# Kernel optimization log

Hardware: AMD Instinct MI355X
Metric: run time of the kernel (lower is better)

The kernel has to match this reference:

```python
import jax, jax.numpy as jnp
import numpy as np

KH = KW = 3
K = KH * KW
GROUPS = 8


def conv_same(x, w, b=None):
    out = jax.lax.conv_general_dilated(x, w, (1, 1), 'SAME',
                                       dimension_numbers=('NHWC', 'HWIO', 'NHWC'))
    if b is not None:
        out = out + b
    return out


def feature_selection(x, w_att, w_sel):
    pooled = x.mean(axis=(1, 2), keepdims=True)            # [B,1,1,C]
    attn = jax.nn.sigmoid(conv_same(pooled, w_att))        # 1x1 conv, sigmoid
    return conv_same(x * (attn + 1.0), w_sel)              # [B,H,W,F]


def deform_sample(x, sy, sx):
    # x: [H,W,G,Cg]; sy,sx: [H,W,G,K] fractional sample coords (zero outside)
    H, W, G, _ = x.shape
    y0 = jnp.floor(sy)
    x0 = jnp.floor(sx)
    wy1 = sy - y0
    wx1 = sx - x0
    gi = jnp.arange(G)[None, None, :, None]

    def gather(yi, xi):
        valid = (yi >= 0) & (yi <= H - 1) & (xi >= 0) & (xi <= W - 1)
        yc = jnp.clip(yi, 0, H - 1).astype(jnp.int32)
        xc = jnp.clip(xi, 0, W - 1).astype(jnp.int32)
        v = x[yc, xc, gi]                                   # [H,W,G,K,Cg]
        return v * valid[..., None]

    v00 = gather(y0, x0)
    v01 = gather(y0, x0 + 1)
    v10 = gather(y0 + 1, x0)
    v11 = gather(y0 + 1, x0 + 1)
    wy1 = wy1[..., None]
    wx1 = wx1[..., None]
    top = v00 * (1 - wx1) + v01 * wx1
    bot = v10 * (1 - wx1) + v11 * wx1
    return top * (1 - wy1) + bot * wy1                      # [H,W,G,K,Cg]


def dcnv2(x, align, w_om, b_om, w_dcn, b_dcn):
    # x: [B,H,W,C] input to deform-conv; align: [B,H,W,Ca] alignment feature
    B, H, W, C = x.shape
    G = GROUPS
    Cg = C // G
    om = conv_same(align, w_om, b_om)                       # [B,H,W,G*3*K]
    off = om[..., :G * 2 * K].reshape(B, H, W, G, K, 2)     # (dy, dx)
    mask = jax.nn.sigmoid(om[..., G * 2 * K:]).reshape(B, H, W, G, K)

    iy = jnp.arange(H, dtype=x.dtype)[:, None, None, None]
    ix = jnp.arange(W, dtype=x.dtype)[None, :, None, None]
    ky, kx = jnp.meshgrid(jnp.arange(KH) - (KH - 1) // 2,
                          jnp.arange(KW) - (KW - 1) // 2, indexing='ij')
    ky = ky.reshape(K).astype(x.dtype)
    kx = kx.reshape(K).astype(x.dtype)
    sy = iy + ky + off[..., 0]                              # [B,H,W,G,K]
    sx = ix + kx + off[..., 1]

    xg = x.reshape(B, H, W, G, Cg)
    sampled = jax.vmap(deform_sample)(xg, sy, sx)           # [B,H,W,G,K,Cg]
    sampled = sampled * mask[..., None]
    sampled = sampled.transpose(0, 1, 2, 4, 3, 5).reshape(B, H, W, K, C)
    wk = w_dcn.reshape(K, C, -1)                            # [K,C,F]
    return jnp.einsum('bhwkc,kcf->bhwf', sampled, wk) + b_dcn


def reference(coarse, fine, w_att, w_sel, w_off, w_om, b_om, w_dcn, b_dcn):
    B, H, W, _ = fine.shape
    coarse_up = jax.image.resize(coarse, (B, H, W, coarse.shape[-1]), 'bilinear')
    fine_cal = feature_selection(fine, w_att, w_sel)
    fc = jnp.concatenate([fine_cal, coarse_up * 2.0], axis=-1)
    align = conv_same(fc, w_off)                            # 1x1, no bias
    aligned = jax.nn.relu(dcnv2(coarse_up, align, w_om, b_om, w_dcn, b_dcn))
    return aligned + fine_cal


def setup_inputs() -> dict:
    key = jax.random.key(0)
    ks = jax.random.split(key, 8)
    B, H, W = 4, 64, 64
    Cc, Cf, F = 256, 256, 256
    s = lambda fan: (2.0 / fan) ** 0.5
    return {
        'coarse': jax.random.normal(ks[0], (B, H // 2, W // 2, Cc), jnp.float32),
        'fine': jax.random.normal(ks[1], (B, H, W, Cf), jnp.float32),
        'w_att': jax.random.normal(ks[2], (1, 1, Cf, Cf), jnp.float32) * s(Cf),
        'w_sel': jax.random.normal(ks[3], (1, 1, Cf, F), jnp.float32) * s(Cf),
        'w_off': jax.random.normal(ks[4], (1, 1, F + Cc, 2 * F), jnp.float32) * s(F + Cc),
        'w_om': jax.random.normal(ks[5], (3, 3, 2 * F, GROUPS * 3 * K), jnp.float32) * 0.01,
        'b_om': jnp.zeros((GROUPS * 3 * K,), jnp.float32),
        'w_dcn': jax.random.normal(ks[6], (3, 3, Cc, F), jnp.float32) * s(9 * Cc),
        'b_dcn': jnp.zeros((F,), jnp.float32),
    }
```

## Files before the change

kernel.cpp:

```cpp
#include <hip/hip_runtime.h>
#include <hip/hip_bf16.h>
#include <cstddef>

constexpr int HWP = 64 * 64;
constexpr int CCH = 256;
constexpr int OMC = 216;
constexpr int KDC = 2304;

typedef __attribute__((ext_vector_type(8))) short bf16x8;
typedef __attribute__((ext_vector_type(4))) float f32x4;

__device__ inline unsigned short f2bf(float x) {
  __hip_bfloat16 h = __float2bfloat16(x);
  return *reinterpret_cast<unsigned short*>(&h);
}
__device__ inline float bf2f(unsigned short u) {
  unsigned int v = ((unsigned int)u) << 16;
  return __uint_as_float(v);
}
__device__ inline void bfpair(unsigned int u, float& a, float& b) {
  a = __uint_as_float(u << 16);
  b = __uint_as_float(u & 0xffff0000u);
}

__global__ __launch_bounds__(256) void prep_transpose(
    const float* __restrict__ w_off, const float* __restrict__ w_om,
    const float* __restrict__ w_sel, const float* __restrict__ w_dcn,
    unsigned short* __restrict__ w_offT, unsigned short* __restrict__ w_omT,
    unsigned short* __restrict__ w_selT, unsigned short* __restrict__ w_dcnT) {
  __shared__ float tile[32][33];
  int bid = blockIdx.x;
  int t = threadIdx.x;
  const float* src;
  unsigned short* dst;
  int in_rs, out_rs, r0, c0, cmax;
  if (bid < 256) {
    int tr = bid >> 4, tc = bid & 15;
    src = w_off; dst = w_offT; in_rs = 512; out_rs = 512;
    r0 = tr * 32; c0 = tc * 32; cmax = 512;
  } else if (bid < 320) {
    int b2 = bid - 256;
    int tr = b2 >> 3, tc = b2 & 7;
    src = w_sel; dst = w_selT; in_rs = 256; out_rs = 256;
    r0 = tr * 32; c0 = tc * 32; cmax = 256;
  } else if (bid < 896) {
    int b2 = bid - 320;
    int tap = b2 >> 6; b2 &= 63;
    int tr = b2 >> 3, tc = b2 & 7;
    src = w_dcn + (size_t)tap * 65536; dst = w_dcnT + (size_t)tap * 65536;
    in_rs = 256; out_rs = 256;
    r0 = tr * 32; c0 = tc * 32; cmax = 256;
  } else {
    int b2 = bid - 896;
    int tap = b2 >> 7; b2 &= 127;
    int tr = b2 >> 3, tc = b2 & 7;
    src = w_om + (size_t)tap * 512 * 216; dst = w_omT + (size_t)tap * 256 * 512;
    in_rs = 216; out_rs = 512;
    r0 = tr * 32; c0 = tc * 32; cmax = 216;
  }
  int row = t >> 3, c4 = (t & 7) * 4;
#pragma unroll
  for (int j = 0; j < 4; ++j) {
    int cc = c0 + c4 + j;
    tile[row][c4 + j] = (cc < cmax) ? src[(size_t)(r0 + row) * in_rs + cc] : 0.f;
  }
  __syncthreads();
  ushort4 v;
  v.x = f2bf(tile[c4 + 0][row]);
  v.y = f2bf(tile[c4 + 1][row]);
  v.z = f2bf(tile[c4 + 2][row]);
  v.w = f2bf(tile[c4 + 3][row]);
  *(ushort4*)&dst[(size_t)(c0 + row) * out_rs + r0 + c4] = v;
}

__global__ __launch_bounds__(256) void pool_partial(
    const float* __restrict__ fine, float* __restrict__ partial) {
  int r = blockIdx.x;
  int b = blockIdx.y;
  int t = threadIdx.x;
  const float* src = fine + ((size_t)b * 4096 + r * 64) * 256 + t;
  float s = 0.f;
#pragma unroll 8
  for (int p = 0; p < 64; ++p) s += src[(size_t)p * 256];
  partial[((size_t)b * 64 + r) * 256 + t] = s;
}

__global__ __launch_bounds__(256) void pool_finish(
    const float* __restrict__ partial, const float* __restrict__ w_att,
    float* __restrict__ scale) {
  __shared__ float pl[256];
  int b = blockIdx.x;
  int t = threadIdx.x;
  const float* pp = partial + (size_t)b * 64 * 256 + t;
  float s = 0.f;
#pragma unroll 8
  for (int r = 0; r < 64; ++r) s += pp[(size_t)r * 256];
  pl[t] = s * (1.0f / 4096.0f);
  __syncthreads();
  float acc = 0.f;
  for (int ci = 0; ci < 256; ++ci) acc += pl[ci] * w_att[ci * 256 + t];
  scale[b * 256 + t] = 1.0f + 1.0f / (1.0f + expf(-acc));
}

__global__ __launch_bounds__(256) void upsample_kernel(
    const float* __restrict__ coarse, unsigned short* __restrict__ upbf,
    unsigned short* __restrict__ alignA) {
  int m = blockIdx.x;
  int c = threadIdx.x;
  int b = m >> 12, h = (m >> 6) & 63, w = m & 63;
  float cy = fminf(fmaxf(h * 0.5f - 0.25f, 0.f), 31.f);
  float cx = fminf(fmaxf(w * 0.5f - 0.25f, 0.f), 31.f);
  int y0 = (int)cy, x0 = (int)cx;
  float fy = cy - y0, fx = cx - x0;
  int y1 = min(y0 + 1, 31), x1 = min(x0 + 1, 31);
  const float* base = coarse + (size_t)b * 32 * 32 * CCH;
  float v00 = base[(y0 * 32 + x0) * CCH + c];
  float v01 = base[(y0 * 32 + x1) * CCH + c];
  float v10 = base[(y1 * 32 + x0) * CCH + c];
  float v11 = base[(y1 * 32 + x1) * CCH + c];
  float top = v00 + (v01 - v00) * fx;
  float bot = v10 + (v11 - v10) * fx;
  float v = top + (bot - top) * fy;
  upbf[(size_t)m * CCH + c] = f2bf(v);
  alignA[(size_t)m * 512 + 256 + c] = f2bf(2.f * v);
}

__global__ __launch_bounds__(256) void gemm_finecal_mfma(
    const float* __restrict__ fine, const float* __restrict__ scale,
    const unsigned short* __restrict__ w_selT,
    float* __restrict__ finecal, unsigned short* __restrict__ alignA) {
  __shared__ unsigned short As[128][72];
  __shared__ unsigned short Bs[64][72];
  __shared__ float sc[256];
  int n0 = blockIdx.x * 64;
  int m0 = blockIdx.y * 128;
  int t = threadIdx.x;
  int wid = t >> 6, lane = t & 63;
  int lrow = lane & 15, lq = lane >> 4;
  int bb = m0 >> 12;
  sc[t] = scale[bb * 256 + t];
  f32x4 acc[2][4];
#pragma unroll
  for (int i = 0; i < 2; ++i)
#pragma unroll
    for (int j = 0; j < 4; ++j) acc[i][j] = (f32x4){0.f, 0.f, 0.f, 0.f};
  for (int k0 = 0; k0 < 256; k0 += 64) {
    __syncthreads();
    for (int u = t; u < 128 * 8; u += 256) {
      int row = u >> 3, ck = u & 7;
      const float* fp = &fine[(size_t)(m0 + row) * 256 + k0 + ck * 8];
      float4 f0 = *(const float4*)fp;
      float4 f1 = *(const float4*)(fp + 4);
      int kb = k0 + ck * 8;
      ushort4 u0 = make_ushort4(f2bf(f0.x * sc[kb]), f2bf(f0.y * sc[kb + 1]),
                                f2bf(f0.z * sc[kb + 2]), f2bf(f0.w * sc[kb + 3]));
      ushort4 u1 = make_ushort4(f2bf(f1.x * sc[kb + 4]), f2bf(f1.y * sc[kb + 5]),
                                f2bf(f1.z * sc[kb + 6]), f2bf(f1.w * sc[kb + 7]));
      *(ushort4*)&As[row][ck * 8] = u0;
      *(ushort4*)&As[row][ck * 8 + 4] = u1;
    }
    for (int u = t; u < 64 * 8; u += 256) {
      int row = u >> 3, ck = u & 7;
      *(uint4*)&Bs[row][ck * 8] = *(const uint4*)&w_selT[(size_t)(n0 + row) * 256 + k0 + ck * 8];
    }
    __syncthreads();
#pragma unroll
    for (int kk = 0; kk < 2; ++kk) {
      bf16x8 a[2], b[4];
#pragma unroll
      for (int mt = 0; mt < 2; ++mt)
        a[mt] = *(const bf16x8*)&As[wid * 32 + mt * 16 + lrow][kk * 32 + lq * 8];
#pragma unroll
      for (int nt = 0; nt < 4; ++nt)
        b[nt] = *(const bf16x8*)&Bs[nt * 16 + lrow][kk * 32 + lq * 8];
#pragma unroll
      for (int mt = 0; mt < 2; ++mt)
#pragma unroll
        for (int nt = 0; nt < 4; ++nt)
          acc[mt][nt] = __builtin_amdgcn_mfma_f32_16x16x32_bf16(
              a[mt], b[nt], acc[mt][nt], 0, 0, 0);
    }
  }
#pragma unroll
  for (int mt = 0; mt < 2; ++mt)
#pragma unroll
    for (int nt = 0; nt < 4; ++nt)
#pragma unroll
      for (int r = 0; r < 4; ++r) {
        int m = m0 + wid * 32 + mt * 16 + lq * 4 + r;
        int n = n0 + nt * 16 + lrow;
        finecal[(size_t)m * 256 + n] = acc[mt][nt][r];
        alignA[(size_t)m * 512 + n] = f2bf(acc[mt][nt][r]);
      }
}

__global__ __launch_bounds__(256) void gemm_align_mfma(
    const unsigned short* __restrict__ alignA,
    const unsigned short* __restrict__ w_offT,
    unsigned short* __restrict__ alignBf) {
  __shared__ unsigned short As[128][72];
  __shared__ unsigned short Bs[64][72];
  int n0 = blockIdx.x * 64;
  int m0 = blockIdx.y * 128;
  int t = threadIdx.x;
  int wid = t >> 6, lane = t & 63;
  int lrow = lane & 15, lq = lane >> 4;
  f32x4 acc[2][4];
#pragma unroll
  for (int i = 0; i < 2; ++i)
#pragma unroll
    for (int j = 0; j < 4; ++j) acc[i][j] = (f32x4){0.f, 0.f, 0.f, 0.f};
  for (int k0 = 0; k0 < 512; k0 += 64) {
    __syncthreads();
    for (int u = t; u < 128 * 8; u += 256) {
      int row = u >> 3, ck = u & 7;
      *(uint4*)&As[row][ck * 8] =
          *(const uint4*)&alignA[(size_t)(m0 + row) * 512 + k0 + ck * 8];
    }
    for (int u = t; u < 64 * 8; u += 256) {
      int row = u >> 3, ck = u & 7;
      *(uint4*)&Bs[row][ck * 8] =
          *(const uint4*)&w_offT[(size_t)(n0 + row) * 512 + k0 + ck * 8];
    }
    __syncthreads();
#pragma unroll
    for (int kk = 0; kk < 2; ++kk) {
      bf16x8 a[2], b[4];
#pragma unroll
      for (int mt = 0; mt < 2; ++mt)
        a[mt] = *(const bf16x8*)&As[wid * 32 + mt * 16 + lrow][kk * 32 + lq * 8];
#pragma unroll
      for (int nt = 0; nt < 4; ++nt)
        b[nt] = *(const bf16x8*)&Bs[nt * 16 + lrow][kk * 32 + lq * 8];
#pragma unroll
      for (int mt = 0; mt < 2; ++mt)
#pragma unroll
        for (int nt = 0; nt < 4; ++nt)
          acc[mt][nt] = __builtin_amdgcn_mfma_f32_16x16x32_bf16(
              a[mt], b[nt], acc[mt][nt], 0, 0, 0);
    }
  }
#pragma unroll
  for (int mt = 0; mt < 2; ++mt)
#pragma unroll
    for (int nt = 0; nt < 4; ++nt)
#pragma unroll
      for (int r = 0; r < 4; ++r) {
        int m = m0 + wid * 32 + mt * 16 + lq * 4 + r;
        int n = n0 + nt * 16 + lrow;
        alignBf[(size_t)m * 512 + n] = f2bf(acc[mt][nt][r]);
      }
}

__global__ __launch_bounds__(256) void om_conv_mfma(
    const unsigned short* __restrict__ alignBf,
    const unsigned short* __restrict__ w_omT,
    const float* __restrict__ b_om,
    float* __restrict__ om) {
  __shared__ unsigned short As[4][66][72];
  __shared__ unsigned short Bs[2][64][72];
  int nblk = blockIdx.x;
  int mblk = blockIdx.y;
  int b = mblk >> 5, hp = mblk & 31;
  int h0 = hp * 2;
  int n0 = nblk * 64;
  int t = threadIdx.x;
  int wid = t >> 6, lane = t & 63;
  int wy = wid >> 1, wx = wid & 1;
  int lrow = lane & 15, lq = lane >> 4;
  const size_t imgbase = (size_t)b * 4096;
  f32x4 acc[4][2];
#pragma unroll
  for (int i = 0; i < 4; ++i)
#pragma unroll
    for (int j = 0; j < 2; ++j) acc[i][j] = (f32x4){0.f, 0.f, 0.f, 0.f};

  auto stageB = [&](int buf, int tap, int c0) {
    for (int u = t; u < 64 * 8; u += 256) {
      int n = u >> 3, ck = u & 7;
      *(uint4*)&Bs[buf][n][ck * 8] =
          *(const uint4*)&w_omT[((size_t)tap * 256 + n0 + n) * 512 + c0 * 64 + ck * 8];
    }
  };
  auto stageA = [&](int c0) {
    for (int u = t; u < 4 * 66 * 8; u += 256) {
      int dy = u / 528;
      int r = u - dy * 528;
      int px = r >> 3, ck = r & 7;
      int w = px - 1;
      int y = h0 - 1 + dy;
      uint4 v = make_uint4(0u, 0u, 0u, 0u);
      if (w >= 0 && w < 64 && y >= 0 && y < 64)
        v = *(const uint4*)&alignBf[(imgbase + y * 64 + w) * 512 + c0 * 64 + ck * 8];
      *(uint4*)&As[dy][px][ck * 8] = v;
    }
  };

  stageB(0, 0, 0);
  stageA(0);
  __syncthreads();
  int buf = 0;
  for (int c0 = 0; c0 < 8; ++c0) {
    for (int tap = 0; tap < 9; ++tap) {
      int ntap = tap + 1, nc0 = c0;
      if (ntap == 9) { ntap = 0; nc0 = (c0 + 1) & 7; }
      stageB(buf ^ 1, ntap, nc0);
      int dyt = tap / 3, dxt = tap - dyt * 3;
#pragma unroll
      for (int kk = 0; kk < 2; ++kk) {
        bf16x8 a[4], bb[2];
#pragma unroll
        for (int mt = 0; mt < 4; ++mt)
          a[mt] = *(const bf16x8*)&As[wy + dyt][mt * 16 + lrow + dxt][kk * 32 + lq * 8];
#pragma unroll
        for (int nt = 0; nt < 2; ++nt)
          bb[nt] = *(const bf16x8*)&Bs[buf][wx * 32 + nt * 16 + lrow][kk * 32 + lq * 8];
#pragma unroll
        for (int mt = 0; mt < 4; ++mt)
#pragma unroll
          for (int nt = 0; nt < 2; ++nt)
            acc[mt][nt] = __builtin_amdgcn_mfma_f32_16x16x32_bf16(
                a[mt], bb[nt], acc[mt][nt], 0, 0, 0);
      }
      __syncthreads();
      buf ^= 1;
    }
    if (c0 < 7) {
      stageA(c0 + 1);
      __syncthreads();
    }
  }
#pragma unroll
  for (int nt = 0; nt < 2; ++nt) {
    int n = n0 + wx * 32 + nt * 16 + lrow;
    if (n < OMC) {
      float bias = b_om[n];
#pragma unroll
      for (int mt = 0; mt < 4; ++mt) {
#pragma unroll
        for (int r = 0; r < 4; ++r) {
          size_t m = imgbase + (size_t)(h0 + wy) * 64 + mt * 16 + lq * 4 + r;
          om[m * OMC + n] = acc[mt][nt][r] + bias;
        }
      }
    }
  }
}

__global__ __launch_bounds__(256) void dcn_sample(
    const float* __restrict__ om, const unsigned short* __restrict__ upbf,
    unsigned short* __restrict__ S, int bh0) {
  __shared__ int offsA[256][4];
  __shared__ float wtsA[256][4];
  int blk = blockIdx.x;
  int bh = bh0 + (blk >> 1);
  int half = blk & 1;
  int b = bh >> 6, h = bh & 63;
  int p0 = half * 32;
  int m0g = bh * 64 + p0;
  int mloc0 = (bh - bh0) * 64 + p0;
  int t = threadIdx.x;
  const unsigned short* upb = upbf + (size_t)b * HWP * CCH;
  int lane = t & 63;
  int ph = t >> 6;
  int c = lane * 4;
  int g = lane >> 3;
  for (int tap = 0; tap < 9; ++tap) {
    int ky = tap / 3, kx = tap - ky * 3;
    __syncthreads();
    {
      int p = t >> 3, gg = t & 7;
      const float* omr = om + (size_t)(m0g + p) * OMC;
      float dy = omr[gg * 18 + tap * 2];
      float dx = omr[gg * 18 + tap * 2 + 1];
      float mk = 1.0f / (1.0f + expf(-omr[144 + gg * 9 + tap]));
      float sy = (float)(h + ky - 1) + dy;
      float sx = (float)(p0 + p + kx - 1) + dx;
      float y0f = floorf(sy), x0f = floorf(sx);
      float fy = sy - y0f, fx = sx - x0f;
      int y0 = (int)y0f, x0 = (int)x0f;
      int y1 = y0 + 1, x1 = x0 + 1;
      float vy0 = (y0 >= 0 && y0 <= 63) ? 1.f : 0.f;
      float vy1 = (y1 >= 0 && y1 <= 63) ? 1.f : 0.f;
      float vx0 = (x0 >= 0 && x0 <= 63) ? 1.f : 0.f;
      float vx1 = (x1 >= 0 && x1 <= 63) ? 1.f : 0.f;
      int yc0 = min(max(y0, 0), 63), yc1 = min(max(y1, 0), 63);
      int xc0 = min(max(x0, 0), 63), xc1 = min(max(x1, 0), 63);
      offsA[t][0] = (yc0 * 64 + xc0) * 256;
      offsA[t][1] = (yc0 * 64 + xc1) * 256;
      offsA[t][2] = (yc1 * 64 + xc0) * 256;
      offsA[t][3] = (yc1 * 64 + xc1) * 256;
      wtsA[t][0] = (1.f - fy) * (1.f - fx) * vy0 * vx0 * mk;
      wtsA[t][1] = (1.f - fy) * fx * vy0 * vx1 * mk;
      wtsA[t][2] = fy * (1.f - fx) * vy1 * vx0 * mk;
      wtsA[t][3] = fy * fx * vy1 * vx1 * mk;
    }
    __syncthreads();
#pragma unroll
    for (int pp = 0; pp < 8; ++pp) {
      int p = ph * 8 + pp;
      int idx = (p << 3) | g;
      int4 o = *(const int4*)&offsA[idx][0];
      float4 wv = *(const float4*)&wtsA[idx][0];
      uint2 u00 = *(const uint2*)&upb[o.x + c];
      uint2 u01 = *(const uint2*)&upb[o.y + c];
      uint2 u10 = *(const uint2*)&upb[o.z + c];
      uint2 u11 = *(const uint2*)&upb[o.w + c];
      float a0, a1, a2, a3, b0, b1, b2, b3, c0, c1, c2, c3, d0, d1, d2, d3;
      bfpair(u00.x, a0, a1); bfpair(u00.y, a2, a3);
      bfpair(u01.x, b0, b1); bfpair(u01.y, b2, b3);
      bfpair(u10.x, c0, c1); bfpair(u10.y, c2, c3);
      bfpair(u11.x, d0, d1); bfpair(u11.y, d2, d3);
      float v0 = wv.x * a0 + wv.y * b0 + wv.z * c0 + wv.w * d0;
      float v1 = wv.x * a1 + wv.y * b1 + wv.z * c1 + wv.w * d1;
      float v2 = wv.x * a2 + wv.y * b2 + wv.z * c2 + wv.w * d2;
      float v3 = wv.x * a3 + wv.y * b3 + wv.z * c3 + wv.w * d3;
      uint2 outv;
      outv.x = (unsigned int)f2bf(v0) | ((unsigned int)f2bf(v1) << 16);
      outv.y = (unsigned int)f2bf(v2) | ((unsigned int)f2bf(v3) << 16);
      *(uint2*)&S[(size_t)(mloc0 + p) * KDC + tap * 256 + c] = outv;
    }
  }
}

__global__ __launch_bounds__(256) void dcn_gemm(
    const unsigned short* __restrict__ S,
    const unsigned short* __restrict__ w_dcnT,
    const float* __restrict__ b_dcn,
    const float* __restrict__ finecal,
    float* __restrict__ outp, int m_base, int kiters) {
  __shared__ unsigned short As[2][64][72];
  __shared__ unsigned short Bs[2][128][72];
  int n0 = blockIdx.x * 128;
  int mloc0 = blockIdx.y * 64;
  int m0 = m_base + mloc0;
  int t = threadIdx.x;
  int wid = t >> 6, lane = t & 63;
  int wy = wid >> 1, wx = wid & 1;
  int lrow = lane & 15, lq = lane >> 4;
  f32x4 acc[2][4];
#pragma unroll
  for (int i = 0; i < 2; ++i)
#pragma unroll
    for (int j = 0; j < 4; ++j) acc[i][j] = (f32x4){0.f, 0.f, 0.f, 0.f};

  int arow = t >> 3, ack = t & 7;
  uint4 pa[2], pb[4];
  auto loadA = [&](int k0, uint4* p) {
#pragma unroll
    for (int i = 0; i < 2; ++i)
      p[i] = *(const uint4*)&S[(size_t)(mloc0 + arow + i * 32) * KDC + k0 + ack * 8];
  };
  auto loadB = [&](int k0, uint4* p) {
    int tap = k0 >> 8, c0 = k0 & 255;
#pragma unroll
    for (int i = 0; i < 4; ++i)
      p[i] = *(const uint4*)&w_dcnT[((size_t)tap * 256 + n0 + arow + i * 32) * 256 + c0 + ack * 8];
  };
  auto storeTiles = [&](int buf, const uint4* a, const uint4* b) {
#pragma unroll
    for (int i = 0; i < 2; ++i)
      *(uint4*)&As[buf][arow + i * 32][ack * 8] = a[i];
#pragma unroll
    for (int i = 0; i < 4; ++i)
      *(uint4*)&Bs[buf][arow + i * 32][ack * 8] = b[i];
  };

  loadA(0, pa);
  loadB(0, pb);
  storeTiles(0, pa, pb);
  __syncthreads();
  int buf = 0;
  for (int kb = 0; kb < kiters; ++kb) {
    bool has_next = (kb + 1) < kiters;
    if (has_next) {
      loadA((kb + 1) * 64, pa);
      loadB((kb + 1) * 64, pb);
    }
#pragma unroll
    for (int kk = 0; kk < 2; ++kk) {
      bf16x8 a[2], b[4];
#pragma unroll
      for (int mt = 0; mt < 2; ++mt)
        a[mt] = *(const bf16x8*)&As[buf][wy * 32 + mt * 16 + lrow][kk * 32 + lq * 8];
#pragma unroll
      for (int nt = 0; nt < 4; ++nt)
        b[nt] = *(const bf16x8*)&Bs[buf][wx * 64 + nt * 16 + lrow][kk * 32 + lq * 8];
#pragma unroll
      for (int mt = 0; mt < 2; ++mt)
#pragma unroll
        for (int nt = 0; nt < 4; ++nt)
          acc[mt][nt] = __builtin_amdgcn_mfma_f32_16x16x32_bf16(
              a[mt], b[nt], acc[mt][nt], 0, 0, 0);
    }
    if (has_next) {
      storeTiles(buf ^ 1, pa, pb);
      __syncthreads();
      buf ^= 1;
    }
  }
#pragma unroll
  for (int mt = 0; mt < 2; ++mt)
#pragma unroll
    for (int nt = 0; nt < 4; ++nt) {
      int f = n0 + wx * 64 + nt * 16 + lrow;
      float bias = b_dcn[f];
#pragma unroll
      for (int r = 0; r < 4; ++r) {
        int m = m0 + wy * 32 + mt * 16 + lq * 4 + r;
        float v = fmaxf(acc[mt][nt][r] + bias, 0.f);
        float fc = __builtin_nontemporal_load(&finecal[(size_t)m * 256 + f]);
        __builtin_nontemporal_store(v + fc, &outp[(size_t)m * 256 + f]);
      }
    }
}

extern "C" void kernel_launch(void* const* d_in, const int* in_sizes, int n_in,
                              void* d_out, int out_size, void* d_ws, size_t ws_size,
                              hipStream_t stream) {
  const float* coarse = (const float*)d_in[0];
  const float* fine   = (const float*)d_in[1];
  const float* w_att  = (const float*)d_in[2];
  const float* w_sel  = (const float*)d_in[3];
  const float* w_off  = (const float*)d_in[4];
  const float* w_om   = (const float*)d_in[5];
  const float* b_om   = (const float*)d_in[6];
  const float* w_dcn  = (const float*)d_in[7];
  const float* b_dcn  = (const float*)d_in[8];
  float* outp = (float*)d_out;

  char* base = (char*)d_ws;
  size_t o = 0;
  float* scale            = (float*)(base + o);          o += 4096;
  float* finecal          = (float*)(base + o);          o += 16777216;
  float* omb              = (float*)(base + o);          o += 14155776;
  unsigned short* upbf    = (unsigned short*)(base + o); o += 8388608;
  unsigned short* w_offT  = (unsigned short*)(base + o); o += 524288;
  unsigned short* w_omT   = (unsigned short*)(base + o); o += 2359296;
  unsigned short* w_selT  = (unsigned short*)(base + o); o += 131072;
  unsigned short* w_dcnT  = (unsigned short*)(base + o); o += 1179648;
  unsigned short* Sbuf    = (unsigned short*)(base + o);
  size_t fixed = o;
  unsigned short* alignA  = Sbuf;
  unsigned short* alignBf = (unsigned short*)((char*)Sbuf + 16777216);
  float* partial = omb;

  bool fullS = (ws_size >= fixed + 75497472);

  prep_transpose<<<dim3(2048), dim3(256), 0, stream>>>(
      w_off, w_om, w_sel, w_dcn, w_offT, w_omT, w_selT, w_dcnT);
  pool_partial<<<dim3(64, 4), dim3(256), 0, stream>>>(fine, partial);
  pool_finish<<<dim3(4), dim3(256), 0, stream>>>(partial, w_att, scale);
  upsample_kernel<<<dim3(16384), dim3(256), 0, stream>>>(coarse, upbf, alignA);
  gemm_finecal_mfma<<<dim3(4, 128), dim3(256), 0, stream>>>(
      fine, scale, w_selT, finecal, alignA);
  gemm_align_mfma<<<dim3(8, 128), dim3(256), 0, stream>>>(alignA, w_offT, alignBf);
  om_conv_mfma<<<dim3(4, 128), dim3(256), 0, stream>>>(alignBf, w_omT, b_om, omb);

  if (fullS) {
    dcn_sample<<<dim3(512), dim3(256), 0, stream>>>(omb, upbf, Sbuf, 0);
    dcn_gemm<<<dim3(2, 256), dim3(256), 0, stream>>>(
        Sbuf, w_dcnT, b_dcn, finecal, outp, 0, KDC / 64);
  } else {
    for (int ch = 0; ch < 2; ++ch) {
      dcn_sample<<<dim3(256), dim3(256), 0, stream>>>(omb, upbf, Sbuf, ch * 128);
      dcn_gemm<<<dim3(2, 128), dim3(256), 0, stream>>>(
          Sbuf, w_dcnT, b_dcn, finecal, outp, ch * 8192, KDC / 64);
    }
  }
}
```

Before: 398.2 us.

## Enlarge align GEMM tile to 128x128 and drop dcn_gemm double buffering

The align GEMM now computes a 128x128 output tile per block, with a 2x2 warp layout and 4x4 MFMA accumulators per wave. This halves the grid and reuses each A tile across twice as many output columns, cutting global traffic for the A operand. Separately, dcn_gemm drops its register-prefetch double buffering and goes back to a single-buffered synchronous load, compute, sync loop. That shrinks LDS use and register pressure, which may allow more resident blocks, but it loses the overlap between global loads and MFMA work.

```diff
diff --git a/kernel.cpp b/kernel.cpp
--- a/kernel.cpp
+++ b/kernel.cpp
@@ -199,15 +199,16 @@
     const unsigned short* __restrict__ w_offT,
     unsigned short* __restrict__ alignBf) {
   __shared__ unsigned short As[128][72];
-  __shared__ unsigned short Bs[64][72];
-  int n0 = blockIdx.x * 64;
+  __shared__ unsigned short Bs[128][72];
+  int n0 = blockIdx.x * 128;
   int m0 = blockIdx.y * 128;
   int t = threadIdx.x;
   int wid = t >> 6, lane = t & 63;
+  int wy = wid >> 1, wx = wid & 1;
   int lrow = lane & 15, lq = lane >> 4;
-  f32x4 acc[2][4];
-#pragma unroll
-  for (int i = 0; i < 2; ++i)
+  f32x4 acc[4][4];
+#pragma unroll
+  for (int i = 0; i < 4; ++i)
 #pragma unroll
     for (int j = 0; j < 4; ++j) acc[i][j] = (f32x4){0.f, 0.f, 0.f, 0.f};
   for (int k0 = 0; k0 < 512; k0 += 64) {
@@ -217,7 +218,7 @@
       *(uint4*)&As[row][ck * 8] =
           *(const uint4*)&alignA[(size_t)(m0 + row) * 512 + k0 + ck * 8];
     }
-    for (int u = t; u < 64 * 8; u += 256) {
+    for (int u = t; u < 128 * 8; u += 256) {
       int row = u >> 3, ck = u & 7;
       *(uint4*)&Bs[row][ck * 8] =
           *(const uint4*)&w_offT[(size_t)(n0 + row) * 512 + k0 + ck * 8];
@@ -225,15 +226,15 @@
     __syncthreads();
 #pragma unroll
     for (int kk = 0; kk < 2; ++kk) {
-      bf16x8 a[2], b[4];
-#pragma unroll
-      for (int mt = 0; mt < 2; ++mt)
-        a[mt] = *(const bf16x8*)&As[wid * 32 + mt * 16 + lrow][kk * 32 + lq * 8];
+      bf16x8 a[4], b[4];
+#pragma unroll
+      for (int mt = 0; mt < 4; ++mt)
+        a[mt] = *(const bf16x8*)&As[wy * 64 + mt * 16 + lrow][kk * 32 + lq * 8];
 #pragma unroll
       for (int nt = 0; nt < 4; ++nt)
-        b[nt] = *(const bf16x8*)&Bs[nt * 16 + lrow][kk * 32 + lq * 8];
-#pragma unroll
-      for (int mt = 0; mt < 2; ++mt)
+        b[nt] = *(const bf16x8*)&Bs[wx * 64 + nt * 16 + lrow][kk * 32 + lq * 8];
+#pragma unroll
+      for (int mt = 0; mt < 4; ++mt)
 #pragma unroll
         for (int nt = 0; nt < 4; ++nt)
           acc[mt][nt] = __builtin_amdgcn_mfma_f32_16x16x32_bf16(
@@ -241,13 +242,13 @@
     }
   }
 #pragma unroll
-  for (int mt = 0; mt < 2; ++mt)
+  for (int mt = 0; mt < 4; ++mt)
 #pragma unroll
     for (int nt = 0; nt < 4; ++nt)
 #pragma unroll
       for (int r = 0; r < 4; ++r) {
-        int m = m0 + wid * 32 + mt * 16 + lq * 4 + r;
-        int n = n0 + nt * 16 + lrow;
+        int m = m0 + wy * 64 + mt * 16 + lq * 4 + r;
+        int n = n0 + wx * 64 + nt * 16 + lrow;
         alignBf[(size_t)m * 512 + n] = f2bf(acc[mt][nt][r]);
       }
 }
@@ -429,8 +430,8 @@
     const float* __restrict__ b_dcn,
     const float* __restrict__ finecal,
     float* __restrict__ outp, int m_base, int kiters) {
-  __shared__ unsigned short As[2][64][72];
-  __shared__ unsigned short Bs[2][128][72];
+  __shared__ unsigned short As[64][72];
+  __shared__ unsigned short Bs[128][72];
   int n0 = blockIdx.x * 128;
   int mloc0 = blockIdx.y * 64;
   int m0 = m_base + mloc0;
@@ -444,59 +445,36 @@
 #pragma unroll
     for (int j = 0; j < 4; ++j) acc[i][j] = (f32x4){0.f, 0.f, 0.f, 0.f};
 
-  int arow = t >> 3, ack = t & 7;
-  uint4 pa[2], pb[4];
-  auto loadA = [&](int k0, uint4* p) {
-#pragma unroll
-    for (int i = 0; i < 2; ++i)
-      p[i] = *(const uint4*)&S[(size_t)(mloc0 + arow + i * 32) * KDC + k0 + ack * 8];
-  };
-  auto loadB = [&](int k0, uint4* p) {
+  for (int kb = 0; kb < kiters; ++kb) {
+    int k0 = kb * 64;
+    __syncthreads();
+    for (int u = t; u < 64 * 8; u += 256) {
+      int row = u >> 3, ck = u & 7;
+      *(uint4*)&As[row][ck * 8] =
+          *(const uint4*)&S[(size_t)(mloc0 + row) * KDC + k0 + ck * 8];
+    }
     int tap = k0 >> 8, c0 = k0 & 255;
-#pragma unroll
-    for (int i = 0; i < 4; ++i)
-      p[i] = *(const uint4*)&w_dcnT[((size_t)tap * 256 + n0 + arow + i * 32) * 256 + c0 + ack * 8];
-  };
-  auto storeTiles = [&](int buf, const uint4* a, const uint4* b) {
-#pragma unroll
-    for (int i = 0; i < 2; ++i)
-      *(uint4*)&As[buf][arow + i * 32][ack * 8] = a[i];
-#pragma unroll
-    for (int i = 0; i < 4; ++i)
-      *(uint4*)&Bs[buf][arow + i * 32][ack * 8] = b[i];
-  };
-
-  loadA(0, pa);
-  loadB(0, pb);
-  storeTiles(0, pa, pb);
-  __syncthreads();
-  int buf = 0;
-  for (int kb = 0; kb < kiters; ++kb) {
-    bool has_next = (kb + 1) < kiters;
-    if (has_next) {
-      loadA((kb + 1) * 64, pa);
-      loadB((kb + 1) * 64, pb);
-    }
+    for (int u = t; u < 128 * 8; u += 256) {
+      int row = u >> 3, ck = u & 7;
+      *(uint4*)&Bs[row][ck * 8] =
+          *(const uint4*)&w_dcnT[((size_t)tap * 256 + n0 + row) * 256 + c0 + ck * 8];
+    }
+    __syncthreads();
 #pragma unroll
     for (int kk = 0; kk < 2; ++kk) {
       bf16x8 a[2], b[4];
 #pragma unroll
       for (int mt = 0; mt < 2; ++mt)
-        a[mt] = *(const bf16x8*)&As[buf][wy * 32 + mt * 16 + lrow][kk * 32 + lq * 8];
+        a[mt] = *(const bf16x8*)&As[wy * 32 + mt * 16 + lrow][kk * 32 + lq * 8];
 #pragma unroll
       for (int nt = 0; nt < 4; ++nt)
-        b[nt] = *(const bf16x8*)&Bs[buf][wx * 64 + nt * 16 + lrow][kk * 32 + lq * 8];
+        b[nt] = *(const bf16x8*)&Bs[wx * 64 + nt * 16 + lrow][kk * 32 + lq * 8];
 #pragma unroll
       for (int mt = 0; mt < 2; ++mt)
 #pragma unroll
         for (int nt = 0; nt < 4; ++nt)
           acc[mt][nt] = __builtin_amdgcn_mfma_f32_16x16x32_bf16(
               a[mt], b[nt], acc[mt][nt], 0, 0, 0);
-    }
-    if (has_next) {
-      storeTiles(buf ^ 1, pa, pb);
-      __syncthreads();
-      buf ^= 1;
     }
   }
 #pragma unroll
@@ -554,7 +532,7 @@
   upsample_kernel<<<dim3(16384), dim3(256), 0, stream>>>(coarse, upbf, alignA);
   gemm_finecal_mfma<<<dim3(4, 128), dim3(256), 0, stream>>>(
       fine, scale, w_selT, finecal, alignA);
-  gemm_align_mfma<<<dim3(8, 128), dim3(256), 0, stream>>>(alignA, w_offT, alignBf);
+  gemm_align_mfma<<<dim3(4, 128), dim3(256), 0, stream>>>(alignA, w_offT, alignBf);
   om_conv_mfma<<<dim3(4, 128), dim3(256), 0, stream>>>(alignBf, w_omT, b_om, omb);
 
   if (fullS) {
```

Result: slower. 418.3 us (+5.0%).
